# Kernel tuning notes

Measured on AMD Instinct MI355X. Metric: run time of the kernel, lower is better.

## Reference

```python
import jax, jax.numpy as jnp
import numpy as np

N = 100000      # nodes
E = 1600000     # edges
F_IN = 128
H = 128
L = 3           # GraphConv layers
C = 47          # classes
EPS = 1e-5      # BatchNorm eps


def setup_inputs() -> dict:
    key = jax.random.key(0)
    ks = jax.random.split(key, 12)
    feat = jax.random.normal(ks[0], (N, F_IN), dtype=jnp.float32)
    src = jax.random.randint(ks[1], (E,), 0, N, dtype=jnp.int32)
    dst = jax.random.randint(ks[2], (E,), 0, N, dtype=jnp.int32)
    s = 0.02
    W_in = jax.random.normal(ks[3], (F_IN, H), dtype=jnp.float32) * s
    b_in = jnp.zeros((H,), dtype=jnp.float32)
    Wc = jax.random.normal(ks[4], (L, H, H), dtype=jnp.float32) * s
    bc = jnp.zeros((L, H), dtype=jnp.float32)
    # BatchNorm (eval mode) params for layers+1 norms
    gamma = jnp.ones((L + 1, H), dtype=jnp.float32)
    beta = jnp.zeros((L + 1, H), dtype=jnp.float32)
    rmean = jax.random.normal(ks[5], (L + 1, H), dtype=jnp.float32) * 0.1
    rvar = jax.random.uniform(ks[6], (L + 1, H), dtype=jnp.float32, minval=0.5, maxval=1.5)
    W_out = jax.random.normal(ks[7], (H, C), dtype=jnp.float32) * s
    b_out = jnp.zeros((C,), dtype=jnp.float32)
    return {"feat": feat, "src": src, "dst": dst, "W_in": W_in, "b_in": b_in,
            "Wc": Wc, "bc": bc, "gamma": gamma, "beta": beta,
            "rmean": rmean, "rvar": rvar, "W_out": W_out, "b_out": b_out}


def _bn(x, g, b, m, v):
    # BatchNorm1d in eval mode (running stats)
    return (x - m) * jax.lax.rsqrt(v + EPS) * g + b


def _degree_norms(src, dst):
    ones = jnp.ones((E,), dtype=jnp.float32)
    deg_out = jax.ops.segment_sum(ones, src, num_segments=N)
    deg_in = jax.ops.segment_sum(ones, dst, num_segments=N)
    norm_src = jax.lax.rsqrt(jnp.maximum(deg_out, 1.0))
    norm_dst = jax.lax.rsqrt(jnp.maximum(deg_in, 1.0))
    return norm_src, norm_dst


def _graph_conv(h, src, dst, norm_src, norm_dst, W, b):
    # DGL GraphConv, norm='both': D_dst^{-1/2} A D_src^{-1/2} H W + b
    h = h * norm_src[:, None]
    agg = jax.ops.segment_sum(h[src], dst, num_segments=N)  # [N, H]
    agg = agg * norm_dst[:, None]
    return agg @ W + b


def reference(feat, src, dst, W_in, b_in, Wc, bc, gamma, beta, rmean, rvar, W_out, b_out):
    norm_src, norm_dst = _degree_norms(src, dst)
    h = feat @ W_in + b_in
    h = jax.nn.relu(_bn(h, gamma[0], beta[0], rmean[0], rvar[0]))
    # dropout is identity in eval mode
    for i in range(L):
        h = _graph_conv(h, src, dst, norm_src, norm_dst, Wc[i], bc[i])
        h = jax.nn.relu(_bn(h, gamma[i + 1], beta[i + 1], rmean[i + 1], rvar[i + 1]))
    return h @ W_out + b_out
```

## Files before the change

kernel.cpp:

```cpp
#include <hip/hip_runtime.h>
#include <cstddef>
#include <cstdint>

#define NN 100000
#define NE 1600000
#define HD 128
#define C_OUT 47
#define EPS_BN 1e-5f
#define SLAB 64
#define SLAB_X 16
#define NXCD 8
#define GEMM0_BLOCKS ((NN + 127) / 128)
#define BUILD_BLOCKS (NE / 256)

typedef _Float16 f16;
typedef __attribute__((ext_vector_type(2))) _Float16 f16x2;
typedef __attribute__((ext_vector_type(8))) _Float16 f16x8;
typedef __attribute__((ext_vector_type(4))) float f32x4;

__device__ inline ushort f16bits(f16 h) { return __builtin_bit_cast(ushort, h); }
__device__ inline uint packf16(f16 a, f16 b) {
  return (uint)f16bits(a) | ((uint)f16bits(b) << 16);
}
__device__ inline uint xcc_id() {
  uint x;
  asm volatile("s_getreg_b32 %0, hwreg(HW_REG_XCC_ID)" : "=s"(x));
  return x & (NXCD - 1);
}

__global__ __launch_bounds__(256) void k_wsplit(
    const float* __restrict__ W_in, const float* __restrict__ Wc,
    const float* __restrict__ W_out,
    uint* __restrict__ wsHi, uint* __restrict__ wsLo) {
  int g = blockIdx.x * 256 + threadIdx.x;
  int m = g >> 13;
  int i = g & 8191;
  int kp = i >> 7, c = i & 127;
  int k = kp << 1;
  int s = kp >> 2, t = kp & 3;
  if (m < 4) {
    const float* W = (m == 0) ? W_in : (Wc + (size_t)(m - 1) * HD * HD);
    float w0 = W[(size_t)k * 128 + c];
    float w1 = W[(size_t)(k + 1) * 128 + c];
    f16 h0 = (f16)w0, h1 = (f16)w1;
    f16 l0 = (f16)(w0 - (float)h0), l1 = (f16)(w1 - (float)h1);
    int idx = m * 8192 + (s * 128 + c) * 4 + t;
    wsHi[idx] = packf16(h0, h1);
    wsLo[idx] = packf16(l0, l1);
  } else if (c < 48) {
    float w0 = (c < C_OUT) ? W_out[(size_t)k * C_OUT + c] : 0.f;
    float w1 = (c < C_OUT) ? W_out[(size_t)(k + 1) * C_OUT + c] : 0.f;
    f16 h0 = (f16)w0, h1 = (f16)w1;
    f16 l0 = (f16)(w0 - (float)h0), l1 = (f16)(w1 - (float)h1);
    int idx = 4 * 8192 + (s * 48 + c) * 4 + t;
    wsHi[idx] = packf16(h0, h1);
    wsLo[idx] = packf16(l0, l1);
  }
}

template <bool A16>
__device__ inline void gemm_body(
    const void* __restrict__ Av, const uint* __restrict__ wHi,
    const uint* __restrict__ wLo, const float* __restrict__ bias,
    const float* __restrict__ gamma, const float* __restrict__ beta,
    const float* __restrict__ rmean, const float* __restrict__ rvar,
    f16* __restrict__ out, int bx) {
  int tid = threadIdx.x;
  int wv = tid >> 6, lane = tid & 63;
  int q = lane >> 4, m16 = lane & 15;
  int row_base = bx * 128 + wv * 32;

  f32x4 acc[2][8];
  #pragma unroll
  for (int mt = 0; mt < 2; ++mt)
    #pragma unroll
    for (int nt = 0; nt < 8; ++nt)
      acc[mt][nt] = (f32x4){0.f, 0.f, 0.f, 0.f};

  #pragma unroll
  for (int kk = 0; kk < 4; ++kk) {
    f16x8 a[2];
    #pragma unroll
    for (int mt = 0; mt < 2; ++mt) {
      int r = row_base + mt * 16 + m16;
      r = r < NN ? r : NN - 1;
      if constexpr (A16) {
        a[mt] = *(const f16x8*)((const f16*)Av + (size_t)r * 128 + kk * 32 + q * 8);
      } else {
        const float4* ap = (const float4*)((const float*)Av + (size_t)r * 128 + kk * 32 + q * 8);
        float4 a0 = ap[0], a1 = ap[1];
        a[mt][0] = (f16)a0.x; a[mt][1] = (f16)a0.y;
        a[mt][2] = (f16)a0.z; a[mt][3] = (f16)a0.w;
        a[mt][4] = (f16)a1.x; a[mt][5] = (f16)a1.y;
        a[mt][6] = (f16)a1.z; a[mt][7] = (f16)a1.w;
      }
    }
    int s = kk * 4 + q;
    #pragma unroll
    for (int nt = 0; nt < 8; ++nt) {
      int n = nt * 16 + m16;
      const f16x8 whi = *(const f16x8*)&wHi[(s * 128 + n) * 4];
      const f16x8 wlo = *(const f16x8*)&wLo[(s * 128 + n) * 4];
      #pragma unroll
      for (int mt = 0; mt < 2; ++mt) {
        acc[mt][nt] = __builtin_amdgcn_mfma_f32_16x16x32_f16(a[mt], whi, acc[mt][nt], 0, 0, 0);
        acc[mt][nt] = __builtin_amdgcn_mfma_f32_16x16x32_f16(a[mt], wlo, acc[mt][nt], 0, 0, 0);
      }
    }
  }

  float s8[8], t8[8];
  #pragma unroll
  for (int nt = 0; nt < 8; ++nt) {
    int col = nt * 16 + m16;
    float sc = gamma[col] * rsqrtf(rvar[col] + EPS_BN);
    s8[nt] = sc;
    t8[nt] = (bias[col] - rmean[col]) * sc + beta[col];
  }
  #pragma unroll
  for (int mt = 0; mt < 2; ++mt) {
    #pragma unroll
    for (int nt = 0; nt < 8; ++nt) {
      int col = nt * 16 + m16;
      #pragma unroll
      for (int e = 0; e < 4; ++e) {
        int r = row_base + mt * 16 + q * 4 + e;
        if (r < NN) {
          float y = fmaxf(acc[mt][nt][e] * s8[nt] + t8[nt], 0.f);
          out[(size_t)r * 128 + col] = (f16)y;
        }
      }
    }
  }
}

__global__ __launch_bounds__(256, 4) void k_mega(
    const int* __restrict__ src, const int* __restrict__ dst,
    int* __restrict__ deg_out_c, int* __restrict__ cursor_c,
    int* __restrict__ slab_c,
    const float* __restrict__ feat, const uint* __restrict__ wsHi,
    const uint* __restrict__ wsLo, const float* __restrict__ b_in,
    const float* __restrict__ gamma, const float* __restrict__ beta,
    const float* __restrict__ rmean, const float* __restrict__ rvar,
    f16* __restrict__ h) {
  if (blockIdx.x >= GEMM0_BLOCKS) {
    int e = (blockIdx.x - GEMM0_BLOCKS) * 256 + threadIdx.x;
    if (e >= NE) return;
    int s = src[e], v = dst[e];
    uint xc = xcc_id();
    __hip_atomic_fetch_add(&deg_out_c[xc * NN + s], 1, __ATOMIC_RELAXED,
                           __HIP_MEMORY_SCOPE_WORKGROUP);
    int pos = __hip_atomic_fetch_add(&cursor_c[xc * NN + v], 1, __ATOMIC_RELAXED,
                                     __HIP_MEMORY_SCOPE_WORKGROUP);
    if (pos < SLAB_X) slab_c[((size_t)xc * NN + v) * SLAB_X + pos] = s;
    return;
  }
  gemm_body<false>(feat, wsHi, wsLo, b_in, gamma, beta, rmean, rvar, h,
                   blockIdx.x);
}

__global__ __launch_bounds__(256) void k_norms(
    const int* __restrict__ deg_out_c, const int* __restrict__ cursor_c,
    int* __restrict__ slab_c, int* __restrict__ deg_in,
    float* __restrict__ norm_src, float* __restrict__ norm_dst) {
  int v = blockIdx.x * blockDim.x + threadIdx.x;
  if (v >= NN) return;
  int d = 0;
  #pragma unroll
  for (int c = 0; c < NXCD; ++c) d += deg_out_c[c * NN + v];
  norm_src[v] = rsqrtf((float)(d > 0 ? d : 1));

  int true_din = 0;
  int tot = 0;
  #pragma unroll
  for (int c = 0; c < NXCD; ++c) {
    int dx = cursor_c[c * NN + v];
    true_din += dx;
    dx = dx < SLAB_X ? dx : SLAB_X;
    const int* seg = slab_c + ((size_t)c * NN + v) * SLAB_X;
    for (int j = 0; j < dx && tot < SLAB; ++j) {
      int val = seg[j];
      slab_c[((size_t)(tot >> 4) * NN + v) * SLAB_X + (tot & 15)] = val;
      ++tot;
    }
  }
  deg_in[v] = tot;
  norm_dst[v] = rsqrtf((float)(true_din > 0 ? true_din : 1));
}

__global__ __launch_bounds__(256) void k_aggregate(
    const f16* __restrict__ h, const int* __restrict__ deg_in,
    const int* __restrict__ slab_c, const float* __restrict__ norm_src,
    const float* __restrict__ norm_dst, f16* __restrict__ agg) {
  int wave = (int)((blockIdx.x * (unsigned)blockDim.x + threadIdx.x) >> 6);
  int lane = threadIdx.x & 63;
  if (wave >= NN) return;
  const f16x2* h2 = (const f16x2*)h;
  const int* base = slab_c + (size_t)wave * SLAB_X;
  int d = deg_in[wave];
  float ax = 0.f, ay = 0.f;
  int j = 0;
  for (; j + 4 <= d; j += 4) {
    int u0 = base[(size_t)((j + 0) >> 4) * NN * SLAB_X + ((j + 0) & 15)];
    int u1 = base[(size_t)((j + 1) >> 4) * NN * SLAB_X + ((j + 1) & 15)];
    int u2 = base[(size_t)((j + 2) >> 4) * NN * SLAB_X + ((j + 2) & 15)];
    int u3 = base[(size_t)((j + 3) >> 4) * NN * SLAB_X + ((j + 3) & 15)];
    float w0 = norm_src[u0], w1 = norm_src[u1];
    float w2 = norm_src[u2], w3 = norm_src[u3];
    f16x2 x0 = h2[(size_t)u0 * 64 + lane];
    f16x2 x1 = h2[(size_t)u1 * 64 + lane];
    f16x2 x2 = h2[(size_t)u2 * 64 + lane];
    f16x2 x3 = h2[(size_t)u3 * 64 + lane];
    ax = fmaf(w0, (float)x0[0], ax); ay = fmaf(w0, (float)x0[1], ay);
    ax = fmaf(w1, (float)x1[0], ax); ay = fmaf(w1, (float)x1[1], ay);
    ax = fmaf(w2, (float)x2[0], ax); ay = fmaf(w2, (float)x2[1], ay);
    ax = fmaf(w3, (float)x3[0], ax); ay = fmaf(w3, (float)x3[1], ay);
  }
  for (; j < d; ++j) {
    int u = base[(size_t)(j >> 4) * NN * SLAB_X + (j & 15)];
    float w = norm_src[u];
    f16x2 x = h2[(size_t)u * 64 + lane];
    ax = fmaf(w, (float)x[0], ax);
    ay = fmaf(w, (float)x[1], ay);
  }
  float nd = norm_dst[wave];
  f16x2 o;
  o[0] = (f16)(ax * nd);
  o[1] = (f16)(ay * nd);
  ((f16x2*)agg)[(size_t)wave * 64 + lane] = o;
}

__global__ __launch_bounds__(256, 4) void k_gemm(
    const f16* __restrict__ A, const uint* __restrict__ wHi,
    const uint* __restrict__ wLo, const float* __restrict__ bias,
    const float* __restrict__ gamma, const float* __restrict__ beta,
    const float* __restrict__ rmean, const float* __restrict__ rvar,
    f16* __restrict__ out) {
  gemm_body<true>(A, wHi, wLo, bias, gamma, beta, rmean, rvar, out, blockIdx.x);
}

__global__ __launch_bounds__(256, 4) void k_gemm_out(
    const f16* __restrict__ A, const uint* __restrict__ wHi,
    const uint* __restrict__ wLo, const float* __restrict__ bias,
    float* __restrict__ out) {
  int tid = threadIdx.x;
  int wv = tid >> 6, lane = tid & 63;
  int q = lane >> 4, m16 = lane & 15;
  int row_base = blockIdx.x * 128 + wv * 32;

  f32x4 acc[2][3];
  #pragma unroll
  for (int mt = 0; mt < 2; ++mt)
    #pragma unroll
    for (int nt = 0; nt < 3; ++nt)
      acc[mt][nt] = (f32x4){0.f, 0.f, 0.f, 0.f};

  #pragma unroll
  for (int kk = 0; kk < 4; ++kk) {
    f16x8 a[2];
    #pragma unroll
    for (int mt = 0; mt < 2; ++mt) {
      int r = row_base + mt * 16 + m16;
      r = r < NN ? r : NN - 1;
      a[mt] = *(const f16x8*)(A + (size_t)r * 128 + kk * 32 + q * 8);
    }
    int s = kk * 4 + q;
    #pragma unroll
    for (int nt = 0; nt < 3; ++nt) {
      int n = nt * 16 + m16;
      const f16x8 whi = *(const f16x8*)&wHi[(s * 48 + n) * 4];
      const f16x8 wlo = *(const f16x8*)&wLo[(s * 48 + n) * 4];
      #pragma unroll
      for (int mt = 0; mt < 2; ++mt) {
        acc[mt][nt] = __builtin_amdgcn_mfma_f32_16x16x32_f16(a[mt], whi, acc[mt][nt], 0, 0, 0);
        acc[mt][nt] = __builtin_amdgcn_mfma_f32_16x16x32_f16(a[mt], wlo, acc[mt][nt], 0, 0, 0);
      }
    }
  }

  #pragma unroll
  for (int nt = 0; nt < 3; ++nt) {
    int col = nt * 16 + m16;
    float b = (col < C_OUT) ? bias[col] : 0.f;
    #pragma unroll
    for (int mt = 0; mt < 2; ++mt) {
      #pragma unroll
      for (int e = 0; e < 4; ++e) {
        int r = row_base + mt * 16 + q * 4 + e;
        if (r < NN && col < C_OUT) {
          out[(size_t)r * C_OUT + col] = acc[mt][nt][e] + b;
        }
      }
    }
  }
}


extern "C" void kernel_launch(void* const* d_in, const int* in_sizes, int n_in,
                              void* d_out, int out_size, void* d_ws, size_t ws_size,
                              hipStream_t stream) {
  const float* feat = (const float*)d_in[0];
  const int* src = (const int*)d_in[1];
  const int* dst = (const int*)d_in[2];
  const float* W_in = (const float*)d_in[3];
  const float* b_in = (const float*)d_in[4];
  const float* Wc = (const float*)d_in[5];
  const float* bc = (const float*)d_in[6];
  const float* gamma = (const float*)d_in[7];
  const float* beta = (const float*)d_in[8];
  const float* rmean = (const float*)d_in[9];
  const float* rvar = (const float*)d_in[10];
  const float* W_out = (const float*)d_in[11];
  const float* b_out = (const float*)d_in[12];
  float* out = (float*)d_out;

  char* p = (char*)d_ws;
  f16* h = (f16*)p;             p += (size_t)NN * HD * sizeof(f16);
  f16* agg = (f16*)p;           p += (size_t)NN * HD * sizeof(f16);
  int* slab_c = (int*)p;        p += (size_t)NXCD * NN * SLAB_X * sizeof(int);
  float* norm_src = (float*)p;  p += (size_t)NN * sizeof(float);
  float* norm_dst = (float*)p;  p += (size_t)NN * sizeof(float);
  int* deg_in = (int*)p;        p += (size_t)NN * sizeof(int);
  uint* wsHi = (uint*)p;        p += (size_t)5 * 8192 * sizeof(uint);
  uint* wsLo = (uint*)p;        p += (size_t)5 * 8192 * sizeof(uint);
  int* deg_out_c = (int*)p;     p += (size_t)NXCD * NN * sizeof(int);
  int* cursor_c = (int*)p;      p += (size_t)NXCD * NN * sizeof(int);

  hipMemsetAsync(deg_out_c, 0, (size_t)2 * NXCD * NN * sizeof(int), stream);

  k_wsplit<<<160, 256, 0, stream>>>(W_in, Wc, W_out, wsHi, wsLo);
  k_mega<<<GEMM0_BLOCKS + BUILD_BLOCKS, 256, 0, stream>>>(
      src, dst, deg_out_c, cursor_c, slab_c, feat, wsHi, wsLo, b_in, gamma,
      beta, rmean, rvar, h);
  k_norms<<<(NN + 255) / 256, 256, 0, stream>>>(deg_out_c, cursor_c, slab_c,
                                                deg_in, norm_src, norm_dst);

  int gblocks = (NN + 127) / 128;
  for (int l = 0; l < 3; ++l) {
    k_aggregate<<<(NN * 64 + 255) / 256, 256, 0, stream>>>(
        h, deg_in, slab_c, norm_src, norm_dst, agg);
    k_gemm<<<gblocks, 256, 0, stream>>>(
        agg, wsHi + (size_t)(l + 1) * 8192, wsLo + (size_t)(l + 1) * 8192,
        bc + (size_t)l * HD,
        gamma + (size_t)(l + 1) * HD, beta + (size_t)(l + 1) * HD,
        rmean + (size_t)(l + 1) * HD, rvar + (size_t)(l + 1) * HD, h);
  }
  k_gemm_out<<<gblocks, 256, 0, stream>>>(
      h, wsHi + (size_t)4 * 8192, wsLo + (size_t)4 * 8192, b_out, out);
}
```

Baseline: 579.6 us.

## Partition edge build by node residue and pack neighbor lists contiguously per node

```diff
diff --git a/kernel.cpp b/kernel.cpp
--- a/kernel.cpp
+++ b/kernel.cpp
@@ -10,8 +10,10 @@
 #define SLAB 64
 #define SLAB_X 16
 #define NXCD 8
+#define NPART 4
 #define GEMM0_BLOCKS ((NN + 127) / 128)
-#define BUILD_BLOCKS (NE / 256)
+#define BPG 1563
+#define BUILD_BLOCKS (NPART * BPG)
 
 typedef _Float16 f16;
 typedef __attribute__((ext_vector_type(2))) _Float16 f16x2;
@@ -134,7 +136,7 @@
   }
 }
 
-__global__ __launch_bounds__(256, 4) void k_mega(
+__global__ __launch_bounds__(256, 8) void k_mega(
     const int* __restrict__ src, const int* __restrict__ dst,
     int* __restrict__ deg_out_c, int* __restrict__ cursor_c,
     int* __restrict__ slab_c,
@@ -144,15 +146,31 @@
     const float* __restrict__ rmean, const float* __restrict__ rvar,
     f16* __restrict__ h) {
   if (blockIdx.x >= GEMM0_BLOCKS) {
-    int e = (blockIdx.x - GEMM0_BLOCKS) * 256 + threadIdx.x;
-    if (e >= NE) return;
-    int s = src[e], v = dst[e];
+    int bb = blockIdx.x - GEMM0_BLOCKS;
+    int g = bb / BPG;
+    int gid = (bb - g * BPG) * 256 + threadIdx.x;
+    int base = gid * 4;
+    if (base >= NE) return;
     uint xc = xcc_id();
-    __hip_atomic_fetch_add(&deg_out_c[xc * NN + s], 1, __ATOMIC_RELAXED,
-                           __HIP_MEMORY_SCOPE_WORKGROUP);
-    int pos = __hip_atomic_fetch_add(&cursor_c[xc * NN + v], 1, __ATOMIC_RELAXED,
-                                     __HIP_MEMORY_SCOPE_WORKGROUP);
-    if (pos < SLAB_X) slab_c[((size_t)xc * NN + v) * SLAB_X + pos] = s;
+    int4 s4 = *(const int4*)(src + base);
+    int4 v4 = *(const int4*)(dst + base);
+    int ss[4], vv[4];
+    *(int4*)ss = s4;
+    *(int4*)vv = v4;
+    #pragma unroll
+    for (int k = 0; k < 4; ++k) {
+      int s = ss[k], v = vv[k];
+      if ((s & (NPART - 1)) == g) {
+        __hip_atomic_fetch_add(&deg_out_c[xc * NN + s], 1, __ATOMIC_RELAXED,
+                               __HIP_MEMORY_SCOPE_WORKGROUP);
+      }
+      if ((v & (NPART - 1)) == g) {
+        int pos = __hip_atomic_fetch_add(&cursor_c[xc * NN + v], 1,
+                                         __ATOMIC_RELAXED,
+                                         __HIP_MEMORY_SCOPE_WORKGROUP);
+        if (pos < SLAB_X) slab_c[((size_t)xc * NN + v) * SLAB_X + pos] = s;
+      }
+    }
     return;
   }
   gemm_body<false>(feat, wsHi, wsLo, b_in, gamma, beta, rmean, rvar, h,
@@ -161,7 +179,8 @@
 
 __global__ __launch_bounds__(256) void k_norms(
     const int* __restrict__ deg_out_c, const int* __restrict__ cursor_c,
-    int* __restrict__ slab_c, int* __restrict__ deg_in,
+    const int* __restrict__ slab_c, int* __restrict__ slab_p,
+    int* __restrict__ deg_in,
     float* __restrict__ norm_src, float* __restrict__ norm_dst) {
   int v = blockIdx.x * blockDim.x + threadIdx.x;
   if (v >= NN) return;
@@ -172,6 +191,7 @@
 
   int true_din = 0;
   int tot = 0;
+  int* dstrow = slab_p + (size_t)v * SLAB;
   #pragma unroll
   for (int c = 0; c < NXCD; ++c) {
     int dx = cursor_c[c * NN + v];
@@ -179,9 +199,7 @@
     dx = dx < SLAB_X ? dx : SLAB_X;
     const int* seg = slab_c + ((size_t)c * NN + v) * SLAB_X;
     for (int j = 0; j < dx && tot < SLAB; ++j) {
-      int val = seg[j];
-      slab_c[((size_t)(tot >> 4) * NN + v) * SLAB_X + (tot & 15)] = val;
-      ++tot;
+      dstrow[tot++] = seg[j];
     }
   }
   deg_in[v] = tot;
@@ -190,21 +208,21 @@
 
 __global__ __launch_bounds__(256) void k_aggregate(
     const f16* __restrict__ h, const int* __restrict__ deg_in,
-    const int* __restrict__ slab_c, const float* __restrict__ norm_src,
+    const int* __restrict__ slab_p, const float* __restrict__ norm_src,
     const float* __restrict__ norm_dst, f16* __restrict__ agg) {
   int wave = (int)((blockIdx.x * (unsigned)blockDim.x + threadIdx.x) >> 6);
   int lane = threadIdx.x & 63;
   if (wave >= NN) return;
   const f16x2* h2 = (const f16x2*)h;
-  const int* base = slab_c + (size_t)wave * SLAB_X;
+  const int* cols = slab_p + (size_t)wave * SLAB;
   int d = deg_in[wave];
   float ax = 0.f, ay = 0.f;
   int j = 0;
   for (; j + 4 <= d; j += 4) {
-    int u0 = base[(size_t)((j + 0) >> 4) * NN * SLAB_X + ((j + 0) & 15)];
-    int u1 = base[(size_t)((j + 1) >> 4) * NN * SLAB_X + ((j + 1) & 15)];
-    int u2 = base[(size_t)((j + 2) >> 4) * NN * SLAB_X + ((j + 2) & 15)];
-    int u3 = base[(size_t)((j + 3) >> 4) * NN * SLAB_X + ((j + 3) & 15)];
+    int u0 = cols[j + 0];
+    int u1 = cols[j + 1];
+    int u2 = cols[j + 2];
+    int u3 = cols[j + 3];
     float w0 = norm_src[u0], w1 = norm_src[u1];
     float w2 = norm_src[u2], w3 = norm_src[u3];
     f16x2 x0 = h2[(size_t)u0 * 64 + lane];
@@ -217,7 +235,7 @@
     ax = fmaf(w3, (float)x3[0], ax); ay = fmaf(w3, (float)x3[1], ay);
   }
   for (; j < d; ++j) {
-    int u = base[(size_t)(j >> 4) * NN * SLAB_X + (j & 15)];
+    int u = cols[j];
     float w = norm_src[u];
     f16x2 x = h2[(size_t)u * 64 + lane];
     ax = fmaf(w, (float)x[0], ax);
@@ -230,7 +248,7 @@
   ((f16x2*)agg)[(size_t)wave * 64 + lane] = o;
 }
 
-__global__ __launch_bounds__(256, 4) void k_gemm(
+__global__ __launch_bounds__(256, 8) void k_gemm(
     const f16* __restrict__ A, const uint* __restrict__ wHi,
     const uint* __restrict__ wLo, const float* __restrict__ bias,
     const float* __restrict__ gamma, const float* __restrict__ beta,
@@ -318,6 +336,7 @@
   f16* h = (f16*)p;             p += (size_t)NN * HD * sizeof(f16);
   f16* agg = (f16*)p;           p += (size_t)NN * HD * sizeof(f16);
   int* slab_c = (int*)p;        p += (size_t)NXCD * NN * SLAB_X * sizeof(int);
+  int* slab_p = (int*)p;        p += (size_t)NN * SLAB * sizeof(int);
   float* norm_src = (float*)p;  p += (size_t)NN * sizeof(float);
   float* norm_dst = (float*)p;  p += (size_t)NN * sizeof(float);
   int* deg_in = (int*)p;        p += (size_t)NN * sizeof(int);
@@ -333,12 +352,13 @@
       src, dst, deg_out_c, cursor_c, slab_c, feat, wsHi, wsLo, b_in, gamma,
       beta, rmean, rvar, h);
   k_norms<<<(NN + 255) / 256, 256, 0, stream>>>(deg_out_c, cursor_c, slab_c,
-                                                deg_in, norm_src, norm_dst);
+                                                slab_p, deg_in, norm_src,
+                                                norm_dst);
 
   int gblocks = (NN + 127) / 128;
   for (int l = 0; l < 3; ++l) {
     k_aggregate<<<(NN * 64 + 255) / 256, 256, 0, stream>>>(
-        h, deg_in, slab_c, norm_src, norm_dst, agg);
+        h, deg_in, slab_p, norm_src, norm_dst, agg);
     k_gemm<<<gblocks, 256, 0, stream>>>(
         agg, wsHi + (size_t)(l + 1) * 8192, wsLo + (size_t)(l + 1) * 8192,
         bc + (size_t)l * HD,
```

Measured after the change: 762.1 us. 31.5% more time.

## Prescale GEMM output by norm_src, compact neighbor lists, two nodes per wave

Applied to the files above, without the earlier changes.

```diff
diff --git a/kernel.cpp b/kernel.cpp
--- a/kernel.cpp
+++ b/kernel.cpp
@@ -64,7 +64,7 @@
     const uint* __restrict__ wLo, const float* __restrict__ bias,
     const float* __restrict__ gamma, const float* __restrict__ beta,
     const float* __restrict__ rmean, const float* __restrict__ rvar,
-    f16* __restrict__ out, int bx) {
+    const float* __restrict__ rowscale, f16* __restrict__ out, int bx) {
   int tid = threadIdx.x;
   int wv = tid >> 6, lane = tid & 63;
   int q = lane >> 4, m16 = lane & 15;
@@ -120,14 +120,16 @@
   #pragma unroll
   for (int mt = 0; mt < 2; ++mt) {
     #pragma unroll
-    for (int nt = 0; nt < 8; ++nt) {
-      int col = nt * 16 + m16;
+    for (int e = 0; e < 4; ++e) {
+      int r = row_base + mt * 16 + q * 4 + e;
+      float rs = 1.f;
+      if (rowscale != nullptr && r < NN) rs = rowscale[r];
       #pragma unroll
-      for (int e = 0; e < 4; ++e) {
-        int r = row_base + mt * 16 + q * 4 + e;
+      for (int nt = 0; nt < 8; ++nt) {
+        int col = nt * 16 + m16;
         if (r < NN) {
           float y = fmaxf(acc[mt][nt][e] * s8[nt] + t8[nt], 0.f);
-          out[(size_t)r * 128 + col] = (f16)y;
+          out[(size_t)r * 128 + col] = (f16)(y * rs);
         }
       }
     }
@@ -155,13 +157,14 @@
     if (pos < SLAB_X) slab_c[((size_t)xc * NN + v) * SLAB_X + pos] = s;
     return;
   }
-  gemm_body<false>(feat, wsHi, wsLo, b_in, gamma, beta, rmean, rvar, h,
-                   blockIdx.x);
+  gemm_body<false>(feat, wsHi, wsLo, b_in, gamma, beta, rmean, rvar, nullptr,
+                   h, blockIdx.x);
 }
 
 __global__ __launch_bounds__(256) void k_norms(
     const int* __restrict__ deg_out_c, const int* __restrict__ cursor_c,
-    int* __restrict__ slab_c, int* __restrict__ deg_in,
+    const int* __restrict__ slab_c, int* __restrict__ slab_p,
+    int* __restrict__ deg_in,
     float* __restrict__ norm_src, float* __restrict__ norm_dst) {
   int v = blockIdx.x * blockDim.x + threadIdx.x;
   if (v >= NN) return;
@@ -172,6 +175,7 @@
 
   int true_din = 0;
   int tot = 0;
+  int* dstrow = slab_p + (size_t)v * SLAB;
   #pragma unroll
   for (int c = 0; c < NXCD; ++c) {
     int dx = cursor_c[c * NN + v];
@@ -179,55 +183,78 @@
     dx = dx < SLAB_X ? dx : SLAB_X;
     const int* seg = slab_c + ((size_t)c * NN + v) * SLAB_X;
     for (int j = 0; j < dx && tot < SLAB; ++j) {
-      int val = seg[j];
-      slab_c[((size_t)(tot >> 4) * NN + v) * SLAB_X + (tot & 15)] = val;
-      ++tot;
+      dstrow[tot++] = seg[j];
     }
   }
   deg_in[v] = tot;
   norm_dst[v] = rsqrtf((float)(true_din > 0 ? true_din : 1));
 }
 
+template <bool SCALED>
 __global__ __launch_bounds__(256) void k_aggregate(
     const f16* __restrict__ h, const int* __restrict__ deg_in,
-    const int* __restrict__ slab_c, const float* __restrict__ norm_src,
+    const int* __restrict__ slab_p, const float* __restrict__ norm_src,
     const float* __restrict__ norm_dst, f16* __restrict__ agg) {
-  int wave = (int)((blockIdx.x * (unsigned)blockDim.x + threadIdx.x) >> 6);
+  int wid = (int)((blockIdx.x * 256u + threadIdx.x) >> 6);
   int lane = threadIdx.x & 63;
-  if (wave >= NN) return;
+  int v0 = wid * 2;
+  if (v0 >= NN) return;
+  int v1 = v0 + 1;
   const f16x2* h2 = (const f16x2*)h;
-  const int* base = slab_c + (size_t)wave * SLAB_X;
-  int d = deg_in[wave];
-  float ax = 0.f, ay = 0.f;
+  const int* c0 = slab_p + (size_t)v0 * SLAB;
+  const int* c1 = slab_p + (size_t)v1 * SLAB;
+  int d0 = deg_in[v0]; d0 = d0 < SLAB ? d0 : SLAB;
+  int d1 = deg_in[v1]; d1 = d1 < SLAB ? d1 : SLAB;
+  float a0x = 0.f, a0y = 0.f, a1x = 0.f, a1y = 0.f;
+  int dmin = d0 < d1 ? d0 : d1;
   int j = 0;
-  for (; j + 4 <= d; j += 4) {
-    int u0 = base[(size_t)((j + 0) >> 4) * NN * SLAB_X + ((j + 0) & 15)];
-    int u1 = base[(size_t)((j + 1) >> 4) * NN * SLAB_X + ((j + 1) & 15)];
-    int u2 = base[(size_t)((j + 2) >> 4) * NN * SLAB_X + ((j + 2) & 15)];
-    int u3 = base[(size_t)((j + 3) >> 4) * NN * SLAB_X + ((j + 3) & 15)];
-    float w0 = norm_src[u0], w1 = norm_src[u1];
-    float w2 = norm_src[u2], w3 = norm_src[u3];
-    f16x2 x0 = h2[(size_t)u0 * 64 + lane];
-    f16x2 x1 = h2[(size_t)u1 * 64 + lane];
-    f16x2 x2 = h2[(size_t)u2 * 64 + lane];
-    f16x2 x3 = h2[(size_t)u3 * 64 + lane];
-    ax = fmaf(w0, (float)x0[0], ax); ay = fmaf(w0, (float)x0[1], ay);
-    ax = fmaf(w1, (float)x1[0], ax); ay = fmaf(w1, (float)x1[1], ay);
-    ax = fmaf(w2, (float)x2[0], ax); ay = fmaf(w2, (float)x2[1], ay);
-    ax = fmaf(w3, (float)x3[0], ax); ay = fmaf(w3, (float)x3[1], ay);
-  }
-  for (; j < d; ++j) {
-    int u = base[(size_t)(j >> 4) * NN * SLAB_X + (j & 15)];
-    float w = norm_src[u];
+  for (; j + 2 <= dmin; j += 2) {
+    int u00 = c0[j], u01 = c0[j + 1];
+    int u10 = c1[j], u11 = c1[j + 1];
+    f16x2 x00 = h2[(size_t)u00 * 64 + lane];
+    f16x2 x01 = h2[(size_t)u01 * 64 + lane];
+    f16x2 x10 = h2[(size_t)u10 * 64 + lane];
+    f16x2 x11 = h2[(size_t)u11 * 64 + lane];
+    if constexpr (SCALED) {
+      a0x += (float)x00[0] + (float)x01[0];
+      a0y += (float)x00[1] + (float)x01[1];
+      a1x += (float)x10[0] + (float)x11[0];
+      a1y += (float)x10[1] + (float)x11[1];
+    } else {
+      float w00 = norm_src[u00], w01 = norm_src[u01];
+      float w10 = norm_src[u10], w11 = norm_src[u11];
+      a0x = fmaf(w00, (float)x00[0], a0x); a0y = fmaf(w00, (float)x00[1], a0y);
+      a0x = fmaf(w01, (float)x01[0], a0x); a0y = fmaf(w01, (float)x01[1], a0y);
+      a1x = fmaf(w10, (float)x10[0], a1x); a1y = fmaf(w10, (float)x10[1], a1y);
+      a1x = fmaf(w11, (float)x11[0], a1x); a1y = fmaf(w11, (float)x11[1], a1y);
+    }
+  }
+  for (int t = j; t < d0; ++t) {
+    int u = c0[t];
     f16x2 x = h2[(size_t)u * 64 + lane];
-    ax = fmaf(w, (float)x[0], ax);
-    ay = fmaf(w, (float)x[1], ay);
-  }
-  float nd = norm_dst[wave];
-  f16x2 o;
-  o[0] = (f16)(ax * nd);
-  o[1] = (f16)(ay * nd);
-  ((f16x2*)agg)[(size_t)wave * 64 + lane] = o;
+    if constexpr (SCALED) {
+      a0x += (float)x[0]; a0y += (float)x[1];
+    } else {
+      float w = norm_src[u];
+      a0x = fmaf(w, (float)x[0], a0x); a0y = fmaf(w, (float)x[1], a0y);
+    }
+  }
+  for (int t = j; t < d1; ++t) {
+    int u = c1[t];
+    f16x2 x = h2[(size_t)u * 64 + lane];
+    if constexpr (SCALED) {
+      a1x += (float)x[0]; a1y += (float)x[1];
+    } else {
+      float w = norm_src[u];
+      a1x = fmaf(w, (float)x[0], a1x); a1y = fmaf(w, (float)x[1], a1y);
+    }
+  }
+  float nd0 = norm_dst[v0], nd1 = norm_dst[v1];
+  f16x2 o0, o1;
+  o0[0] = (f16)(a0x * nd0); o0[1] = (f16)(a0y * nd0);
+  o1[0] = (f16)(a1x * nd1); o1[1] = (f16)(a1y * nd1);
+  ((f16x2*)agg)[(size_t)v0 * 64 + lane] = o0;
+  ((f16x2*)agg)[(size_t)v1 * 64 + lane] = o1;
 }
 
 __global__ __launch_bounds__(256, 4) void k_gemm(
@@ -235,8 +262,9 @@
     const uint* __restrict__ wLo, const float* __restrict__ bias,
     const float* __restrict__ gamma, const float* __restrict__ beta,
     const float* __restrict__ rmean, const float* __restrict__ rvar,
-    f16* __restrict__ out) {
-  gemm_body<true>(A, wHi, wLo, bias, gamma, beta, rmean, rvar, out, blockIdx.x);
+    const float* __restrict__ rowscale, f16* __restrict__ out) {
+  gemm_body<true>(A, wHi, wLo, bias, gamma, beta, rmean, rvar, rowscale, out,
+                  blockIdx.x);
 }
 
 __global__ __launch_bounds__(256, 4) void k_gemm_out(
@@ -318,6 +346,7 @@
   f16* h = (f16*)p;             p += (size_t)NN * HD * sizeof(f16);
   f16* agg = (f16*)p;           p += (size_t)NN * HD * sizeof(f16);
   int* slab_c = (int*)p;        p += (size_t)NXCD * NN * SLAB_X * sizeof(int);
+  int* slab_p = (int*)p;        p += (size_t)NN * SLAB * sizeof(int);
   float* norm_src = (float*)p;  p += (size_t)NN * sizeof(float);
   float* norm_dst = (float*)p;  p += (size_t)NN * sizeof(float);
   int* deg_in = (int*)p;        p += (size_t)NN * sizeof(int);
@@ -333,17 +362,25 @@
       src, dst, deg_out_c, cursor_c, slab_c, feat, wsHi, wsLo, b_in, gamma,
       beta, rmean, rvar, h);
   k_norms<<<(NN + 255) / 256, 256, 0, stream>>>(deg_out_c, cursor_c, slab_c,
-                                                deg_in, norm_src, norm_dst);
+                                                slab_p, deg_in, norm_src,
+                                                norm_dst);
 
   int gblocks = (NN + 127) / 128;
+  int ablocks = (NN / 2 * 64 + 255) / 256;
   for (int l = 0; l < 3; ++l) {
-    k_aggregate<<<(NN * 64 + 255) / 256, 256, 0, stream>>>(
-        h, deg_in, slab_c, norm_src, norm_dst, agg);
+    if (l == 0) {
+      k_aggregate<false><<<ablocks, 256, 0, stream>>>(
+          h, deg_in, slab_p, norm_src, norm_dst, agg);
+    } else {
+      k_aggregate<true><<<ablocks, 256, 0, stream>>>(
+          h, deg_in, slab_p, norm_src, norm_dst, agg);
+    }
+    const float* rs = (l < 2) ? norm_src : nullptr;
     k_gemm<<<gblocks, 256, 0, stream>>>(
         agg, wsHi + (size_t)(l + 1) * 8192, wsLo + (size_t)(l + 1) * 8192,
         bc + (size_t)l * HD,
         gamma + (size_t)(l + 1) * HD, beta + (size_t)(l + 1) * HD,
-        rmean + (size_t)(l + 1) * HD, rvar + (size_t)(l + 1) * HD, h);
+        rmean + (size_t)(l + 1) * HD, rvar + (size_t)(l + 1) * HD, rs, h);
   }
   k_gemm_out<<<gblocks, 256, 0, stream>>>(
       h, wsHi + (size_t)4 * 8192, wsLo + (size_t)4 * 8192, b_out, out);
```

Result: slower. 609.4 us (+5.1%).
